# Kernel optimization log

Measured on AMD Instinct MI355X. Metric: run time of the kernel, lower is better.

## Reference

```python
import jax, jax.numpy as jnp
import numpy as np

B, C_IN, T, H, W = 32, 1024, 7, 14, 14
C_INTER = 512


def setup_inputs() -> dict:
    key = jax.random.key(0)
    ks = jax.random.split(key, 8)
    s = lambda fan_in: 1.0 / np.sqrt(fan_in)
    return {
        "x_window": jax.random.normal(ks[0], (B, C_IN, T, H, W), jnp.float32),
        "nodes": jax.random.normal(ks[1], (T, C_INTER), jnp.float32),
        "Wq": jax.random.normal(ks[2], (C_IN, C_INTER), jnp.float32) * s(C_IN),
        "bq": jnp.zeros((C_INTER,), jnp.float32),
        "Wk": jax.random.normal(ks[3], (C_INTER, C_INTER), jnp.float32) * s(C_INTER),
        "bk": jnp.zeros((C_INTER,), jnp.float32),
        "Wv": jax.random.normal(ks[4], (C_IN, C_INTER), jnp.float32) * s(C_IN),
        "bv": jnp.zeros((C_INTER,), jnp.float32),
        "Wo": jax.random.normal(ks[5], (C_INTER, C_IN), jnp.float32) * s(C_INTER),
        "bo": jnp.zeros((C_IN,), jnp.float32),
    }


def reference(x_window, nodes, Wq, bq, Wk, bk, Wv, bv, Wo, bo):
    # x_window: (B, C_in, T, H, W); dropout is identity at eval time.
    t_mid = x_window.shape[2] // 2
    x_item = x_window[:, :, t_mid]                                   # (B, C_in, H, W)
    # pointwise (Linear3d) projections over channel dim
    query = jnp.einsum("bchw,cd->bdhw", x_item, Wq) + bq[None, :, None, None]
    key = nodes @ Wk + bk                                            # (T, C_inter)
    value = jnp.einsum("bcthw,cd->bdthw", x_window, Wv) + bv[None, :, None, None, None]
    # per-pixel attention scores over the T node keys
    alpha = jnp.einsum("bdhw,td->bthw", query, key)                  # (B, T, H, W)
    alpha = jax.nn.softmax(alpha, axis=1)
    # per-pixel weighted temporal sum
    y = jnp.einsum("bthw,bdthw->bdhw", alpha, value)                 # (B, C_inter, H, W)
    out = jnp.einsum("bdhw,dc->bchw", y, Wo) + bo[None, :, None, None]
    return out[:, :, None]                                           # (B, C_in, 1, H, W)
```

## Files before the change

kernel.cpp:

```cpp
#include <hip/hip_runtime.h>
#include <hip/hip_bf16.h>
#include <stdint.h>

#define BB    32
#define CIN   1024
#define TT    7
#define HHWW  196
#define HW4   49
#define CI    512
#define TMID  3
#define MM    (BB*HHWW)
#define NCH   16
#define CSZ   64

using bf16 = __hip_bfloat16;
typedef __attribute__((ext_vector_type(8))) short short8;
typedef __attribute__((ext_vector_type(4))) short s16x4;
typedef __attribute__((ext_vector_type(4))) float f32x4;

__device__ __forceinline__ void gload_lds16(const void* g, void* l) {
    __builtin_amdgcn_global_load_lds((const __attribute__((address_space(1))) void*)g,
                                     (__attribute__((address_space(3))) void*)l, 16, 0, 0);
}

template <int EPI>
__device__ __forceinline__ void gemm_body(const bf16* __restrict__ A, const bf16* __restrict__ Bt,
                                          void* __restrict__ Cout, const float* __restrict__ bias,
                                          int M, int N, int K, int bm, int bn,
                                          bf16* As, bf16* Bs) {
    int tid = threadIdx.x;
    int wid = tid >> 6, lane = tid & 63;
    int wr = wid >> 1, wc = wid & 1;
    f32x4 acc[4][4] = {};
    const bf16* Ab = A + (size_t)bm * 128 * K;
    const bf16* Bb = Bt + (size_t)bn * 128 * K;
    int row = lane & 15;
    int sw = row & 7;

    auto stage = [&](int buf, int k0) {
        #pragma unroll
        for (int it = 0; it < 4; ++it) {
            int g = it * 256 + tid;
            int r = g >> 3;
            int src8 = (g & 7) ^ (r & 7);
            gload_lds16(Ab + (size_t)r * K + k0 + src8 * 8, &As[buf * 8192 + g * 8]);
            gload_lds16(Bb + (size_t)r * K + k0 + src8 * 8, &Bs[buf * 8192 + g * 8]);
        }
    };

    stage(0, 0);
    int cur = 0;
    for (int k0 = 0; k0 < K; k0 += 64) {
        if (k0 + 64 < K) {
            stage(cur ^ 1, k0 + 64);
            asm volatile("s_waitcnt vmcnt(8)" ::: "memory");
        } else {
            asm volatile("s_waitcnt vmcnt(0)" ::: "memory");
        }
        __builtin_amdgcn_s_barrier();
        bf16* Ac = &As[cur * 8192];
        bf16* Bc = &Bs[cur * 8192];
        #pragma unroll
        for (int kk = 0; kk < 2; ++kk) {
            int kb8 = kk * 4 + (lane >> 4);
            int rd8 = kb8 ^ sw;
            short8 a[4], b[4];
            #pragma unroll
            for (int mi = 0; mi < 4; ++mi) {
                int arow = wr * 64 + mi * 16 + row;
                a[mi] = *(const short8*)&Ac[(arow * 8 + rd8) * 8];
            }
            #pragma unroll
            for (int ni = 0; ni < 4; ++ni) {
                int brow = wc * 64 + ni * 16 + row;
                b[ni] = *(const short8*)&Bc[(brow * 8 + rd8) * 8];
            }
            #pragma unroll
            for (int mi = 0; mi < 4; ++mi)
                #pragma unroll
                for (int ni = 0; ni < 4; ++ni)
                    acc[mi][ni] = __builtin_amdgcn_mfma_f32_16x16x32_bf16(a[mi], b[ni], acc[mi][ni], 0, 0, 0);
        }
        __builtin_amdgcn_s_barrier();
        cur ^= 1;
    }

    int col_l = lane & 15, row_l = (lane >> 4) * 4;
    if constexpr (EPI == 0) {
        bf16* C = (bf16*)Cout;
        #pragma unroll
        for (int mi = 0; mi < 4; ++mi) {
            int row0 = bm * 128 + wr * 64 + mi * 16 + row_l;
            #pragma unroll
            for (int ni = 0; ni < 4; ++ni) {
                int col = bn * 128 + wc * 64 + ni * 16 + col_l;
                #pragma unroll
                for (int r = 0; r < 4; ++r)
                    C[(size_t)(row0 + r) * N + col] = __float2bfloat16(acc[mi][ni][r]);
            }
        }
    } else {
        float* Cf = (float*)Cout;
        #pragma unroll
        for (int ni = 0; ni < 4; ++ni) {
            int n = bn * 128 + wc * 64 + ni * 16 + col_l;
            float bz = bias[n];
            #pragma unroll
            for (int mi = 0; mi < 4; ++mi) {
                int m0 = bm * 128 + wr * 64 + mi * 16 + row_l;
                int b = m0 / HHWW;
                int hw0 = m0 - b * HHWW;
                f32x4 v = acc[mi][ni];
                v[0] += bz; v[1] += bz; v[2] += bz; v[3] += bz;
                *(f32x4*)&Cf[((size_t)b * CIN + n) * HHWW + hw0] = v;
            }
        }
    }
}

__global__ __launch_bounds__(256) void k_prep1(
    const float* __restrict__ nodes, const float* __restrict__ Wk, const float* __restrict__ bk,
    float* __restrict__ key,
    const float* __restrict__ Wv, const float* __restrict__ Wo,
    bf16* __restrict__ Wv_bf, bf16* __restrict__ WoT_bf,
    const float* __restrict__ bv, const float* __restrict__ bo, float* __restrict__ bvo) {
    __shared__ __align__(16) float lds[64 * 65];
    int u = blockIdx.x, tid = threadIdx.x;
    if (u < 56) {
        int t = u >> 3, dc = u & 7;
        int d_l = tid & 63, q = tid >> 6;
        int d = dc * 64 + d_l;
        float acc = 0.f;
        const float* nr = nodes + t * CI;
        #pragma unroll 4
        for (int c = q * 128; c < q * 128 + 128; ++c)
            acc = fmaf(nr[c], Wk[(size_t)c * CI + d], acc);
        lds[q * 64 + d_l] = acc;
        __syncthreads();
        if (q == 0)
            key[t * CI + d] = lds[d_l] + lds[64 + d_l] + lds[128 + d_l] + lds[192 + d_l] + bk[d];
    } else if (u < 568) {
        int i4 = ((u - 56) * 256 + tid) * 4;
        f32x4 v = *(const f32x4*)&Wv[i4];
        s16x4 o;
        #pragma unroll
        for (int j = 0; j < 4; ++j) { bf16 h = __float2bfloat16(v[j]); o[j] = *(short*)&h; }
        *(s16x4*)&Wv_bf[i4] = o;
    } else if (u < 696) {
        int u3 = u - 568;
        int dt = u3 >> 4, ct = u3 & 15;
        int r0 = tid >> 6, c = tid & 63;
        #pragma unroll
        for (int k = 0; k < 16; ++k) {
            int r = k * 4 + r0;
            lds[r * 65 + c] = Wo[(size_t)(dt * 64 + r) * CIN + ct * 64 + c];
        }
        __syncthreads();
        #pragma unroll
        for (int k = 0; k < 16; ++k) {
            int r = k * 4 + r0;
            WoT_bf[(size_t)(ct * 64 + r) * CI + dt * 64 + c] = __float2bfloat16(lds[c * 65 + r]);
        }
    } else {
        int cp0 = (u - 696) * 32;
        int cp_l = tid & 31, dq = tid >> 5;
        float acc = 0.f;
        #pragma unroll 4
        for (int d = dq * 64; d < dq * 64 + 64; ++d)
            acc = fmaf(bv[d], Wo[(size_t)d * CIN + cp0 + cp_l], acc);
        lds[dq * 32 + cp_l] = acc;
        __syncthreads();
        if (dq == 0) {
            float v = bo[cp0 + cp_l];
            #pragma unroll
            for (int g = 0; g < 8; ++g) v += lds[g * 32 + cp_l];
            bvo[cp0 + cp_l] = v;
        }
    }
}

__global__ __launch_bounds__(256) void k_prep2(
    const bf16* __restrict__ WoT_bf, const bf16* __restrict__ Wv_bf, bf16* __restrict__ WvoT,
    const float* __restrict__ Wq, const float* __restrict__ bq,
    const float* __restrict__ key, float* __restrict__ Wqk, float* __restrict__ bqk) {
    __shared__ __align__(16) bf16 As[2 * 128 * 64];
    __shared__ __align__(16) bf16 Bs[2 * 128 * 64];
    int bid = blockIdx.x;
    if (bid < 64) {
        gemm_body<0>(WoT_bf, Wv_bf, (void*)WvoT, nullptr, 1024, 1024, 512, bid >> 3, bid & 7, As, Bs);
        return;
    }
    int c = (bid - 64) * 4 + (threadIdx.x >> 6);
    int lane = threadIdx.x & 63;
    if (c > CIN) return;
    const float* src = (c < CIN) ? (Wq + (size_t)c * CI) : bq;
    float acc[TT] = {};
    #pragma unroll 2
    for (int it = 0; it < CI / 64; ++it) {
        float w = src[it * 64 + lane];
        #pragma unroll
        for (int t = 0; t < TT; ++t) acc[t] = fmaf(w, key[t * CI + it * 64 + lane], acc[t]);
    }
    #pragma unroll
    for (int t = 0; t < TT; ++t) {
        float v = acc[t];
        for (int off = 32; off; off >>= 1) v += __shfl_down(v, off);
        if (lane == 0) { if (c < CIN) Wqk[c * 8 + t] = v; else bqk[t] = v; }
    }
}

__global__ __launch_bounds__(256) void k_alpha(const float* __restrict__ x,
                                               const float* __restrict__ Wqk,
                                               float* __restrict__ part) {
    __shared__ float wq_s[CSZ * 8];
    int ch = blockIdx.x, b = blockIdx.y;
    int tid = threadIdx.x;
    for (int i = tid; i < CSZ * 8; i += 256) wq_s[i] = Wqk[ch * CSZ * 8 + i];
    __syncthreads();
    if (tid < HHWW) {
        float acc[TT] = {};
        const float* xb = x + (size_t)(b * CIN + ch * CSZ) * TT * HHWW + TMID * HHWW + tid;
        #pragma unroll 8
        for (int c = 0; c < CSZ; ++c) {
            float v = xb[(size_t)c * TT * HHWW];
            #pragma unroll
            for (int t = 0; t < TT; ++t) acc[t] = fmaf(v, wq_s[c * 8 + t], acc[t]);
        }
        #pragma unroll
        for (int t = 0; t < TT; ++t)
            part[((size_t)(b * NCH + ch) * TT + t) * HHWW + tid] = acc[t];
    }
}

__global__ __launch_bounds__(256) void k_softmaxF(const float* __restrict__ part,
                                                  const float* __restrict__ bqk,
                                                  float* __restrict__ alphaF) {
    int b = blockIdx.x;
    int tid = threadIdx.x;
    if (tid >= HHWW) return;
    float s[TT];
    #pragma unroll
    for (int t = 0; t < TT; ++t) s[t] = bqk[t];
    #pragma unroll
    for (int ch = 0; ch < NCH; ++ch)
        #pragma unroll
        for (int t = 0; t < TT; ++t)
            s[t] += part[((size_t)(b * NCH + ch) * TT + t) * HHWW + tid];
    float mx = s[0];
    #pragma unroll
    for (int t = 1; t < TT; ++t) mx = fmaxf(mx, s[t]);
    float e[TT], sum = 0.f;
    #pragma unroll
    for (int t = 0; t < TT; ++t) { e[t] = __expf(s[t] - mx); sum += e[t]; }
    float inv = 1.f / sum;
    #pragma unroll
    for (int t = 0; t < TT; ++t) alphaF[(size_t)b * TT * HHWW + t * HHWW + tid] = e[t] * inv;
}

__global__ __launch_bounds__(256) void k_smxw(const float* __restrict__ x,
                                              const float* __restrict__ alphaF,
                                              bf16* __restrict__ xw) {
    __shared__ __align__(16) float al[TT * HHWW];
    __shared__ __align__(16) bf16 txp[HHWW * 32];
    int c0 = blockIdx.x * 32;
    int b = blockIdx.y;
    int tid = threadIdx.x;
    for (int i = tid; i < TT * HHWW; i += 256) al[i] = alphaF[(size_t)b * TT * HHWW + i];
    __syncthreads();
    const f32x4* xp = (const f32x4*)x;
    f32x4 acc[7] = {};
    #pragma unroll
    for (int t = 0; t < TT; ++t) {
        #pragma unroll
        for (int k = 0; k < 7; ++k) {
            int w = k * 256 + tid;
            if (k == 6 && w >= 1568) continue;
            int c_l = w / 49;
            int hw4 = w - c_l * 49;
            f32x4 a4 = *(const f32x4*)&al[t * HHWW + hw4 * 4];
            f32x4 xv = xp[((size_t)(b * CIN + c0 + c_l) * TT + t) * HW4 + hw4];
            acc[k] += a4 * xv;
        }
    }
    #pragma unroll
    for (int k = 0; k < 7; ++k) {
        int w = k * 256 + tid;
        if (k == 6 && w >= 1568) continue;
        int c_l = w / 49;
        int hw4 = w - c_l * 49;
        int v = (hw4 & 7) << 2;
        #pragma unroll
        for (int r = 0; r < 4; ++r)
            txp[(hw4 * 4 + r) * 32 + (c_l ^ v)] = __float2bfloat16(acc[k][r]);
    }
    __syncthreads();
    #pragma unroll
    for (int k = 0; k < 7; ++k) {
        int w = k * 256 + tid;
        if (k == 6 && w >= 1568) continue;
        int m = w >> 3, seg = w & 7;
        int v = ((m >> 2) & 7) << 2;
        s16x4 val = *(const s16x4*)&txp[m * 32 + ((seg * 4) ^ v)];
        *(s16x4*)&xw[(size_t)(b * HHWW + m) * CIN + c0 + seg * 4] = val;
    }
}

__global__ __launch_bounds__(256) void k_gemm1(const bf16* __restrict__ A, const bf16* __restrict__ Bt,
                                               float* __restrict__ C, const float* __restrict__ bias) {
    __shared__ __align__(16) bf16 As[2 * 128 * 64];
    __shared__ __align__(16) bf16 Bs[2 * 128 * 64];
    gemm_body<1>(A, Bt, (void*)C, bias, MM, CIN, CIN, blockIdx.x, blockIdx.y, As, Bs);
}

extern "C" void kernel_launch(void* const* d_in, const int* in_sizes, int n_in,
                              void* d_out, int out_size, void* d_ws, size_t ws_size,
                              hipStream_t stream) {
    const float* x     = (const float*)d_in[0];
    const float* nodes = (const float*)d_in[1];
    const float* Wq    = (const float*)d_in[2];
    const float* bq    = (const float*)d_in[3];
    const float* Wk    = (const float*)d_in[4];
    const float* bk    = (const float*)d_in[5];
    const float* Wv    = (const float*)d_in[6];
    const float* bv    = (const float*)d_in[7];
    const float* Wo    = (const float*)d_in[8];
    const float* bo    = (const float*)d_in[9];

    uint8_t* w = (uint8_t*)d_ws;
    size_t off = 0;
    auto alloc = [&](size_t bytes) -> void* {
        void* p = w + off;
        off = (off + bytes + 255) & ~(size_t)255;
        return p;
    };
    float* key    = (float*)alloc((size_t)TT * CI * 4);
    float* Wqk    = (float*)alloc((size_t)CIN * 8 * 4);
    float* bqk    = (float*)alloc(8 * 4);
    float* bvo    = (float*)alloc((size_t)CIN * 4);
    bf16*  Wv_bf  = (bf16*)alloc((size_t)CIN * CI * 2);
    bf16*  WoT_bf = (bf16*)alloc((size_t)CIN * CI * 2);
    bf16*  WvoT   = (bf16*)alloc((size_t)CIN * CIN * 2);
    float* part   = (float*)alloc((size_t)BB * NCH * TT * HHWW * 4);
    float* alphaF = (float*)alloc((size_t)BB * TT * HHWW * 4);
    bf16*  xw     = (bf16*)alloc((size_t)MM * CIN * 2);
    (void)ws_size;

    k_prep1<<<728, 256, 0, stream>>>(nodes, Wk, bk, key, Wv, Wo, Wv_bf, WoT_bf, bv, bo, bvo);
    k_prep2<<<321, 256, 0, stream>>>(WoT_bf, Wv_bf, WvoT, Wq, bq, key, Wqk, bqk);
    k_alpha<<<dim3(NCH, BB), 256, 0, stream>>>(x, Wqk, part);
    k_softmaxF<<<BB, 256, 0, stream>>>(part, bqk, alphaF);
    k_smxw<<<dim3(32, BB), 256, 0, stream>>>(x, alphaF, xw);
    k_gemm1<<<dim3(49, 8), 256, 0, stream>>>(xw, WvoT, (float*)d_out, bvo);
}
```

Baseline: 90.08 us.

## Move Wv·Wo weight GEMM into smxw kernel using smaller 64x64 tiles

The WvoT weight-product GEMM (1024x1024x512) is moved out of k_prep2 and into the same launch as the alpha-weighted temporal reduction. It now runs as 256 blocks of 64x64 tiles alongside the 1024 smxw blocks. The GEMM was on the critical path before k_alpha and softmax, even though only the final GEMM needs it. Running it concurrently with the bandwidth-bound smxw work is meant to hide its cost. In exchange the tiles are smaller with single-buffered LDS, and LDS is shared through one 18KB buffer, which may reduce occupancy of the smxw blocks.

```diff
diff --git a/kernel.cpp b/kernel.cpp
--- a/kernel.cpp
+++ b/kernel.cpp
@@ -114,6 +114,64 @@
                 v[0] += bz; v[1] += bz; v[2] += bz; v[3] += bz;
                 *(f32x4*)&Cf[((size_t)b * CIN + n) * HHWW + hw0] = v;
             }
+        }
+    }
+}
+
+__device__ __forceinline__ void gemm0_small(const bf16* __restrict__ A, const bf16* __restrict__ Bt,
+                                            bf16* __restrict__ C, int bm, int bn, char* smem) {
+    bf16* As = (bf16*)smem;
+    bf16* Bs = (bf16*)(smem + 8192);
+    const int K = 512, N = 1024;
+    int tid = threadIdx.x;
+    int wid = tid >> 6, lane = tid & 63;
+    int wr = wid >> 1, wc = wid & 1;
+    f32x4 acc[2][2] = {};
+    const bf16* Ab = A + (size_t)bm * 64 * K;
+    const bf16* Bb = Bt + (size_t)bn * 64 * K;
+    int row = lane & 15;
+    int sw = row & 7;
+
+    for (int k0 = 0; k0 < K; k0 += 64) {
+        #pragma unroll
+        for (int it = 0; it < 2; ++it) {
+            int g = it * 256 + tid;
+            int r = g >> 3;
+            int src8 = (g & 7) ^ (r & 7);
+            gload_lds16(Ab + (size_t)r * K + k0 + src8 * 8, &As[g * 8]);
+            gload_lds16(Bb + (size_t)r * K + k0 + src8 * 8, &Bs[g * 8]);
+        }
+        __syncthreads();
+        #pragma unroll
+        for (int kk = 0; kk < 2; ++kk) {
+            int kb8 = kk * 4 + (lane >> 4);
+            int rd8 = kb8 ^ sw;
+            short8 a[2], b[2];
+            #pragma unroll
+            for (int mi = 0; mi < 2; ++mi)
+                a[mi] = *(const short8*)&As[((wr * 32 + mi * 16 + row) * 8 + rd8) * 8];
+            #pragma unroll
+            for (int ni = 0; ni < 2; ++ni)
+                b[ni] = *(const short8*)&Bs[((wc * 32 + ni * 16 + row) * 8 + rd8) * 8];
+            #pragma unroll
+            for (int mi = 0; mi < 2; ++mi)
+                #pragma unroll
+                for (int ni = 0; ni < 2; ++ni)
+                    acc[mi][ni] = __builtin_amdgcn_mfma_f32_16x16x32_bf16(a[mi], b[ni], acc[mi][ni], 0, 0, 0);
+        }
+        __syncthreads();
+    }
+
+    int col_l = lane & 15, row_l = (lane >> 4) * 4;
+    #pragma unroll
+    for (int mi = 0; mi < 2; ++mi) {
+        int row0 = bm * 64 + wr * 32 + mi * 16 + row_l;
+        #pragma unroll
+        for (int ni = 0; ni < 2; ++ni) {
+            int col = bn * 64 + wc * 32 + ni * 16 + col_l;
+            #pragma unroll
+            for (int r = 0; r < 4; ++r)
+                C[(size_t)(row0 + r) * N + col] = __float2bfloat16(acc[mi][ni][r]);
         }
     }
 }
@@ -179,18 +237,10 @@
     }
 }
 
-__global__ __launch_bounds__(256) void k_prep2(
-    const bf16* __restrict__ WoT_bf, const bf16* __restrict__ Wv_bf, bf16* __restrict__ WvoT,
+__global__ __launch_bounds__(256) void k_wqk(
     const float* __restrict__ Wq, const float* __restrict__ bq,
     const float* __restrict__ key, float* __restrict__ Wqk, float* __restrict__ bqk) {
-    __shared__ __align__(16) bf16 As[2 * 128 * 64];
-    __shared__ __align__(16) bf16 Bs[2 * 128 * 64];
-    int bid = blockIdx.x;
-    if (bid < 64) {
-        gemm_body<0>(WoT_bf, Wv_bf, (void*)WvoT, nullptr, 1024, 1024, 512, bid >> 3, bid & 7, As, Bs);
-        return;
-    }
-    int c = (bid - 64) * 4 + (threadIdx.x >> 6);
+    int c = blockIdx.x * 4 + (threadIdx.x >> 6);
     int lane = threadIdx.x & 63;
     if (c > CIN) return;
     const float* src = (c < CIN) ? (Wq + (size_t)c * CI) : bq;
@@ -257,14 +307,20 @@
     for (int t = 0; t < TT; ++t) alphaF[(size_t)b * TT * HHWW + t * HHWW + tid] = e[t] * inv;
 }
 
-__global__ __launch_bounds__(256) void k_smxw(const float* __restrict__ x,
-                                              const float* __restrict__ alphaF,
-                                              bf16* __restrict__ xw) {
-    __shared__ __align__(16) float al[TT * HHWW];
-    __shared__ __align__(16) bf16 txp[HHWW * 32];
-    int c0 = blockIdx.x * 32;
-    int b = blockIdx.y;
-    int tid = threadIdx.x;
+__global__ __launch_bounds__(256) void k_smxwg0(
+    const float* __restrict__ x, const float* __restrict__ alphaF, bf16* __restrict__ xw,
+    const bf16* __restrict__ WoT_bf, const bf16* __restrict__ Wv_bf, bf16* __restrict__ WvoT) {
+    __shared__ __align__(16) char smem[18048];
+    int bid = blockIdx.x, tid = threadIdx.x;
+    if (bid < 256) {
+        gemm0_small(WoT_bf, Wv_bf, WvoT, bid >> 4, bid & 15, smem);
+        return;
+    }
+    float* al = (float*)smem;
+    bf16* txp = (bf16*)(smem + 5504);
+    int u = bid - 256;
+    int c0 = (u & 31) * 32;
+    int b = u >> 5;
     for (int i = tid; i < TT * HHWW; i += 256) al[i] = alphaF[(size_t)b * TT * HHWW + i];
     __syncthreads();
     const f32x4* xp = (const f32x4*)x;
@@ -346,9 +402,9 @@
     (void)ws_size;
 
     k_prep1<<<728, 256, 0, stream>>>(nodes, Wk, bk, key, Wv, Wo, Wv_bf, WoT_bf, bv, bo, bvo);
-    k_prep2<<<321, 256, 0, stream>>>(WoT_bf, Wv_bf, WvoT, Wq, bq, key, Wqk, bqk);
+    k_wqk<<<257, 256, 0, stream>>>(Wq, bq, key, Wqk, bqk);
     k_alpha<<<dim3(NCH, BB), 256, 0, stream>>>(x, Wqk, part);
     k_softmaxF<<<BB, 256, 0, stream>>>(part, bqk, alphaF);
-    k_smxw<<<dim3(32, BB), 256, 0, stream>>>(x, alphaF, xw);
+    k_smxwg0<<<1280, 256, 0, stream>>>(x, alphaF, xw, WoT_bf, Wv_bf, WvoT);
     k_gemm1<<<dim3(49, 8), 256, 0, stream>>>(xw, WvoT, (float*)d_out, bvo);
 }
```

Result: faster. 88.10 us (median of 3 runs) (-2.2%).
